# Kernel optimization log

Measured on AMD Instinct MI355X. Metric: run time of the kernel, lower is better.

The kernel has to match this reference:

```python
import jax, jax.numpy as jnp
import numpy as np

N, E, G = 50000, 800000, 64
IN, EDGE = 128, 16
HID, H = 32, 4
FHID, HF = 64, 4
OUT = 16
NEG_SLOPE = 0.2


def _segment_softmax(logits, seg, num):
    m = jax.ops.segment_max(logits, seg, num_segments=num)
    m = jnp.where(jnp.isfinite(m), m, 0.0)
    p = jnp.exp(logits - m[seg])
    s = jax.ops.segment_sum(p, seg, num_segments=num)
    return p / (s[seg] + 1e-16)


def gatv2(x, src, dst, eattr, Wl, bl, Wr, br, We, att, bias, concat):
    # PyG GATv2Conv with add_self_loops=True (edge_attr fill_value='mean')
    n = x.shape[0]
    heads, ch = att.shape
    ones = jnp.ones((src.shape[0],), x.dtype)
    cnt = jax.ops.segment_sum(ones, dst, num_segments=n)
    mean_attr = jax.ops.segment_sum(eattr, dst, num_segments=n) / jnp.maximum(cnt, 1.0)[:, None]
    loop = jnp.arange(n)
    s = jnp.concatenate([src, loop])
    d = jnp.concatenate([dst, loop])
    ea = jnp.concatenate([eattr, mean_attr], axis=0)
    xl = (x @ Wl + bl).reshape(n, heads, ch)   # lin_l (source)
    xr = (x @ Wr + br).reshape(n, heads, ch)   # lin_r (target)
    ee = (ea @ We).reshape(-1, heads, ch)      # lin_edge (no bias)
    z = jax.nn.leaky_relu(xl[s] + xr[d] + ee, NEG_SLOPE)  # [E+N, H, C]
    logits = jnp.einsum('ehc,hc->eh', z, att)
    alpha = _segment_softmax(logits, d, n)
    out = jax.ops.segment_sum(alpha[:, :, None] * xl[s], d, num_segments=n)  # [N, H, C]
    out = out.reshape(n, heads * ch) if concat else out.mean(axis=1)
    return out + bias


def _forward(x, edge_attr, src, dst, batch,
             Wl0, bl0, Wr0, br0, We0, att0, bo0,
             Wlh, blh, Wrh, brh, Weh, atth, boh,
             Wlf, blf, Wrf, brf, Wef, attf, bof,
             Wlin, blin):
    h1 = jax.nn.relu(gatv2(x, src, dst, edge_attr, Wl0, bl0, Wr0, br0, We0, att0, bo0, True))
    h2 = jax.nn.relu(gatv2(h1, src, dst, edge_attr, Wlh, blh, Wrh, brh, Weh, atth, boh, True))
    h3 = jax.nn.relu(gatv2(h2, src, dst, edge_attr, Wlf, blf, Wrf, brf, Wef, attf, bof, False))
    # global_mean_pool over graphs
    gsum = jax.ops.segment_sum(h3, batch, num_segments=G)
    gcnt = jax.ops.segment_sum(jnp.ones((h3.shape[0],), h3.dtype), batch, num_segments=G)
    g = gsum / jnp.maximum(gcnt, 1.0)[:, None]
    return g @ Wlin + blin  # final_dropout inactive in eval mode


def setup_inputs():
    key = jax.random.key(0)
    ks = jax.random.split(key, 20)
    def p(i, shape, fan_in):
        return jax.random.normal(ks[i], shape, jnp.float32) / np.sqrt(fan_in)
    z = lambda *s: jnp.zeros(s, jnp.float32)
    return {
        'x': jax.random.normal(ks[0], (N, IN), jnp.float32),
        'edge_index': jax.random.randint(ks[1], (2, E), 0, N),
        'batch': jnp.sort(jax.random.randint(ks[2], (N,), 0, G)),
        'edge_attr': jax.random.normal(ks[3], (E, EDGE), jnp.float32),
        'Wl0': p(4, (IN, H * HID), IN), 'bl0': z(H * HID),
        'Wr0': p(5, (IN, H * HID), IN), 'br0': z(H * HID),
        'We0': p(6, (EDGE, H * HID), EDGE), 'att0': p(7, (H, HID), HID), 'bo0': z(H * HID),
        'Wlh': p(8, (H * HID, H * HID), H * HID), 'blh': z(H * HID),
        'Wrh': p(9, (H * HID, H * HID), H * HID), 'brh': z(H * HID),
        'Weh': p(10, (EDGE, H * HID), EDGE), 'atth': p(11, (H, HID), HID), 'boh': z(H * HID),
        'Wlf': p(12, (H * HID, HF * FHID), H * HID), 'blf': z(HF * FHID),
        'Wrf': p(13, (H * HID, HF * FHID), H * HID), 'brf': z(HF * FHID),
        'Wef': p(14, (EDGE, HF * FHID), EDGE), 'attf': p(15, (HF, FHID), FHID), 'bof': z(FHID),
        'Wlin': p(16, (FHID, OUT), FHID), 'blin': z(OUT),
    }


def reference(x, edge_index, batch, edge_attr, Wl0, bl0, Wr0, br0, We0, att0, bo0, Wlh, blh, Wrh, brh, Weh, atth, boh, Wlf, blf, Wrf, brf, Wef, attf, bof, Wlin, blin):
    return _forward(x, edge_attr, edge_index[0], edge_index[1], batch,
                    Wl0, bl0, Wr0, br0, We0, att0, bo0,
                    Wlh, blh, Wrh, brh, Weh, atth, boh,
                    Wlf, blf, Wrf, brf, Wef, attf, bof,
                    Wlin, blin)
```

## Files before the change

### kernel.cpp

```cpp
#include <hip/hip_runtime.h>
#include <cstddef>

#define NSLOPE 0.2f

constexpr int NN = 50000;
constexpr int EE = 800000;
constexpr int GG = 64;
constexpr int SCAN_B = 1024;

typedef unsigned short ushort_t;
typedef __bf16 bhalf;
typedef bhalf bhalf8 __attribute__((ext_vector_type(8)));
typedef float floatx4 __attribute__((ext_vector_type(4)));

__device__ __forceinline__ ushort_t f2b(float f) {
  unsigned int u = __float_as_uint(f);
  unsigned int r = (u + 0x7fffu + ((u >> 16) & 1u)) >> 16;
  return (ushort_t)r;
}
__device__ __forceinline__ float b2f(ushort_t b) {
  return __uint_as_float(((unsigned int)b) << 16);
}

__global__ void hist_kernel(const int* __restrict__ dst, int* __restrict__ hist, int E) {
  int e = blockIdx.x * blockDim.x + threadIdx.x;
  if (e < E) atomicAdd(&hist[dst[e]], 1);
}

__global__ void scan_block_kernel(const int* __restrict__ in, int* __restrict__ out,
                                  int* __restrict__ bsum, int n) {
  __shared__ int tmp[SCAN_B];
  int gid = blockIdx.x * SCAN_B + threadIdx.x;
  int v = (gid < n) ? in[gid] : 0;
  tmp[threadIdx.x] = v;
  __syncthreads();
  for (int off = 1; off < SCAN_B; off <<= 1) {
    int t = (threadIdx.x >= off) ? tmp[threadIdx.x - off] : 0;
    __syncthreads();
    tmp[threadIdx.x] += t;
    __syncthreads();
  }
  if (gid < n) out[gid] = tmp[threadIdx.x];
  if (threadIdx.x == SCAN_B - 1) bsum[blockIdx.x] = tmp[threadIdx.x];
}

__global__ void scan_totals_kernel(const int* __restrict__ bsum, int* __restrict__ boff, int nb) {
  if (blockIdx.x == 0 && threadIdx.x == 0) {
    int run = 0;
    for (int i = 0; i < nb; ++i) { boff[i] = run; run += bsum[i]; }
  }
}

__global__ void add_offsets_kernel(int* __restrict__ rowptr, const int* __restrict__ boff, int n) {
  int gid = blockIdx.x * SCAN_B + threadIdx.x;
  if (gid == 0) rowptr[0] = 0;
  if (gid < n) rowptr[1 + gid] += boff[blockIdx.x];
}

__global__ void copy_cursor_kernel(const int* __restrict__ rowptr, int* __restrict__ cursor, int n) {
  int i = blockIdx.x * blockDim.x + threadIdx.x;
  if (i < n) cursor[i] = rowptr[i];
}

__global__ void scatter_perm_kernel(const int* __restrict__ dst, int* __restrict__ cursor,
                                    int* __restrict__ perm, int E) {
  int e = blockIdx.x * blockDim.x + threadIdx.x;
  if (e < E) {
    int pos = atomicAdd(&cursor[dst[e]], 1);
    perm[pos] = e;
  }
}

__global__ void permute_kernel(const int* __restrict__ perm, const int* __restrict__ src,
                               const float* __restrict__ eattr,
                               int* __restrict__ srcp, float* __restrict__ eap, int E) {
  int j = blockIdx.x * blockDim.x + threadIdx.x;
  if (j >= E) return;
  int e = perm[j];
  srcp[j] = src[e];
  const float4* a = reinterpret_cast<const float4*>(eattr + (size_t)e * 16);
  float4* b = reinterpret_cast<float4*>(eap + (size_t)j * 16);
  b[0] = a[0]; b[1] = a[1]; b[2] = a[2]; b[3] = a[3];
}

__global__ void mean_attr_kernel(const int* __restrict__ rowptr, const float* __restrict__ eap,
                                 const int* __restrict__ perm, const float* __restrict__ eattr,
                                 int usePerm, float* __restrict__ meanattr, int N) {
  int idx = blockIdx.x * blockDim.x + threadIdx.x;
  if (idx >= N * 16) return;
  int i = idx >> 4, k = idx & 15;
  int beg = rowptr[i], end = rowptr[i + 1];
  float acc = 0.f;
  if (usePerm) {
    for (int j = beg; j < end; ++j) acc += eattr[(size_t)perm[j] * 16 + k];
  } else {
    for (int j = beg; j < end; ++j) acc += eap[(size_t)j * 16 + k];
  }
  int c = end - beg; if (c < 1) c = 1;
  meanattr[idx] = acc / (float)c;
}

__global__ void f2b_kernel(const float* __restrict__ in, ushort_t* __restrict__ out, int n4) {
  int i = blockIdx.x * blockDim.x + threadIdx.x;
  if (i >= n4) return;
  float4 v = reinterpret_cast<const float4*>(in)[i];
  ushort4 o = make_ushort4(f2b(v.x), f2b(v.y), f2b(v.z), f2b(v.w));
  reinterpret_cast<ushort4*>(out)[i] = o;
}

__global__ void prep_w_kernel(const float* W0, ushort_t* T0, int n0,
                              const float* W1, ushort_t* T1, int n1,
                              const float* W2, ushort_t* T2, int n2,
                              const float* W3, ushort_t* T3, int n3,
                              const float* W4, ushort_t* T4, int n4,
                              const float* W5, ushort_t* T5, int n5) {
  const float* W; ushort_t* T; int Nc;
  switch (blockIdx.y) {
    case 0: W = W0; T = T0; Nc = n0; break;
    case 1: W = W1; T = T1; Nc = n1; break;
    case 2: W = W2; T = T2; Nc = n2; break;
    case 3: W = W3; T = T3; Nc = n3; break;
    case 4: W = W4; T = T4; Nc = n4; break;
    default: W = W5; T = T5; Nc = n5; break;
  }
  int idx = blockIdx.x * blockDim.x + threadIdx.x;
  if (idx >= Nc * 128) return;
  int n = idx >> 7, k = idx & 127;
  T[idx] = f2b(W[(size_t)k * Nc + n]);
}

__global__ __launch_bounds__(256) void gemm_bt_dual_bf16(
    const ushort_t* __restrict__ Xb,
    const ushort_t* __restrict__ Wt0, const float* __restrict__ b0, ushort_t* __restrict__ Y0,
    const ushort_t* __restrict__ Wt1, const float* __restrict__ b1, ushort_t* __restrict__ Y1,
    int M, int Nc) {
  constexpr int K = 128, BM = 128, BN = 128, LDT = 136;
  __shared__ ushort_t Als[BM * LDT];
  __shared__ ushort_t Bls[BN * LDT];
  int nb = Nc >> 7;
  int half = blockIdx.y / nb;
  int cb = blockIdx.y % nb;
  const ushort_t* Wt = half ? Wt1 : Wt0;
  const float* bias = half ? b1 : b0;
  ushort_t* Y = half ? Y1 : Y0;
  int r0 = blockIdx.x * BM;
  int col0 = cb * BN;
  int tid = threadIdx.x;
  {
    int rl = tid >> 5;
    int kq = (tid & 31) * 4;
#pragma unroll
    for (int s = 0; s < 16; ++s) {
      int row = rl + s * 8;
      int grow = r0 + row;
      ushort4 v = make_ushort4(0, 0, 0, 0);
      if (grow < M) v = *reinterpret_cast<const ushort4*>(Xb + (size_t)grow * K + kq);
      *reinterpret_cast<ushort4*>(&Als[row * LDT + kq]) = v;
      ushort4 wv = *reinterpret_cast<const ushort4*>(Wt + (size_t)(col0 + row) * K + kq);
      *reinterpret_cast<ushort4*>(&Bls[row * LDT + kq]) = wv;
    }
  }
  __syncthreads();
  int lane = tid & 63;
  int w = tid >> 6;
  int m0 = (w >> 1) * 64;
  int n0 = (w & 1) * 64;
  int rin = lane & 15, quad = lane >> 4;
  floatx4 acc[4][4];
#pragma unroll
  for (int i = 0; i < 4; ++i)
#pragma unroll
    for (int j = 0; j < 4; ++j) acc[i][j] = (floatx4){0.f, 0.f, 0.f, 0.f};
#pragma unroll
  for (int kt = 0; kt < 4; ++kt) {
    int ko = kt * 32 + quad * 8;
    bhalf8 af[4], bf[4];
#pragma unroll
    for (int i = 0; i < 4; ++i)
      af[i] = *reinterpret_cast<const bhalf8*>(&Als[(m0 + i * 16 + rin) * LDT + ko]);
#pragma unroll
    for (int i = 0; i < 4; ++i)
      bf[i] = *reinterpret_cast<const bhalf8*>(&Bls[(n0 + i * 16 + rin) * LDT + ko]);
#pragma unroll
    for (int mi = 0; mi < 4; ++mi)
#pragma unroll
      for (int ni = 0; ni < 4; ++ni)
        acc[mi][ni] = __builtin_amdgcn_mfma_f32_16x16x32_bf16(af[mi], bf[ni], acc[mi][ni], 0, 0, 0);
  }
#pragma unroll
  for (int ni = 0; ni < 4; ++ni) {
    int gcol = col0 + n0 + ni * 16 + rin;
    float bb = bias[gcol];
#pragma unroll
    for (int mi = 0; mi < 4; ++mi) {
      int growb = r0 + m0 + mi * 16 + quad * 4;
#pragma unroll
      for (int r = 0; r < 4; ++r) {
        int grow = growb + r;
        if (grow < M) Y[(size_t)grow * Nc + gcol] = f2b(acc[mi][ni][r] + bb);
      }
    }
  }
}

template <int VPL>
__device__ __forceinline__ void loadb(const ushort_t* p, float* v) {
  if constexpr (VPL == 2) {
    ushort2 t = *reinterpret_cast<const ushort2*>(p);
    v[0] = b2f(t.x); v[1] = b2f(t.y);
  } else {
    ushort4 t = *reinterpret_cast<const ushort4*>(p);
    v[0] = b2f(t.x); v[1] = b2f(t.y); v[2] = b2f(t.z); v[3] = b2f(t.w);
  }
}
template <int VPL>
__device__ __forceinline__ void storeb(ushort_t* p, const float* v) {
  if constexpr (VPL == 2) {
    *reinterpret_cast<ushort2*>(p) = make_ushort2(f2b(v[0]), f2b(v[1]));
  } else {
    *reinterpret_cast<ushort4*>(p) = make_ushort4(f2b(v[0]), f2b(v[1]), f2b(v[2]), f2b(v[3]));
  }
}

template <int VPL>
__device__ __forceinline__ float lrelu_dot(const float* xv, const float* rv,
                                           const float (*wreg)[VPL], const float* areg,
                                           const float* ea) {
  float part = 0.f;
#pragma unroll
  for (int j = 0; j < VPL; ++j) {
    float z = xv[j] + rv[j];
#pragma unroll
    for (int k = 0; k < 16; ++k) z = fmaf(ea[k], wreg[k][j], z);
    z = (z > 0.f) ? z : NSLOPE * z;
    part = fmaf(z, areg[j], part);
  }
  part += __shfl_xor(part, 1);
  part += __shfl_xor(part, 2);
  part += __shfl_xor(part, 4);
  part += __shfl_xor(part, 8);
  return part;
}

template <int EB, int VPL, int C>
__device__ __forceinline__ void process_group(
    const int* __restrict__ srcp, const float* __restrict__ eap, int j,
    const ushort_t* __restrict__ xl, int lane, const float* rv,
    const float (*wreg)[VPL], const float* areg,
    float& m, float& s, float* acc) {
  int sn[EB];
#pragma unroll
  for (int u = 0; u < EB; ++u) sn[u] = srcp[j + u];
  float xv[EB][VPL];
#pragma unroll
  for (int u = 0; u < EB; ++u) loadb<VPL>(xl + (size_t)sn[u] * C + lane * VPL, xv[u]);
  float lg[EB];
#pragma unroll
  for (int u = 0; u < EB; ++u) {
    const float* ap = eap + (size_t)(j + u) * 16;
    float ea[16];
#pragma unroll
    for (int k = 0; k < 16; ++k) ea[k] = ap[k];
    lg[u] = lrelu_dot<VPL>(xv[u], rv, wreg, areg, ea);
  }
  float newm = m;
#pragma unroll
  for (int u = 0; u < EB; ++u) newm = fmaxf(newm, lg[u]);
  float sc = __expf(m - newm);
  float p[EB], ps = 0.f;
#pragma unroll
  for (int u = 0; u < EB; ++u) { p[u] = __expf(lg[u] - newm); ps += p[u]; }
  s = fmaf(s, sc, ps);
#pragma unroll
  for (int jj = 0; jj < VPL; ++jj) {
    float t = p[0] * xv[0][jj];
#pragma unroll
    for (int u = 1; u < EB; ++u) t = fmaf(p[u], xv[u][jj], t);
    acc[jj] = fmaf(acc[jj], sc, t);
  }
  m = newm;
}

template <int VPL, int C>
__device__ __forceinline__ void process_one(
    int sn, const float* ea,
    const ushort_t* __restrict__ xl, int lane, const float* rv,
    const float (*wreg)[VPL], const float* areg,
    float& m, float& s, float* acc) {
  float xv[VPL];
  loadb<VPL>(xl + (size_t)sn * C + lane * VPL, xv);
  float lg = lrelu_dot<VPL>(xv, rv, wreg, areg, ea);
  float newm = fmaxf(m, lg);
  float sc = __expf(m - newm);
  float p = __expf(lg - newm);
  s = fmaf(s, sc, p);
#pragma unroll
  for (int jj = 0; jj < VPL; ++jj) acc[jj] = fmaf(acc[jj], sc, p * xv[jj]);
  m = newm;
}

template <int C, bool FINAL>
__global__ __launch_bounds__(256) void gat_fused_kernel(
    const int* __restrict__ rowptr,
    const int* __restrict__ srcp, const float* __restrict__ eap,
    const int* __restrict__ perm, const int* __restrict__ src,
    const float* __restrict__ eattr, const float* __restrict__ meanattr,
    int usePerm,
    const ushort_t* __restrict__ xl, const ushort_t* __restrict__ xr,
    const float* __restrict__ We,
    const float* __restrict__ att,
    const float* __restrict__ bias, ushort_t* __restrict__ hout, int N) {
  constexpr int VPL = C / 64;
  constexpr int EB = 4;
  const int lane = threadIdx.x & 63;
  int d = __builtin_amdgcn_readfirstlane(blockIdx.x * (blockDim.x >> 6) + (threadIdx.x >> 6));
  if (d >= N) return;

  float wreg[16][VPL];
  float areg[VPL];
#pragma unroll
  for (int k = 0; k < 16; ++k)
#pragma unroll
    for (int j = 0; j < VPL; ++j) wreg[k][j] = We[k * C + lane * VPL + j];
#pragma unroll
  for (int j = 0; j < VPL; ++j) areg[j] = att[lane * VPL + j];

  int beg = rowptr[d], end = rowptr[d + 1];
  float rv[VPL];
  loadb<VPL>(xr + (size_t)d * C + lane * VPL, rv);

  float m = -INFINITY, s = 0.f;
  float acc[VPL];
#pragma unroll
  for (int j = 0; j < VPL; ++j) acc[j] = 0.f;

  if (!usePerm) {
    int j = beg;
    for (; j + EB <= end; j += EB)
      process_group<EB, VPL, C>(srcp, eap, j, xl, lane, rv, wreg, areg, m, s, acc);
    for (; j < end; ++j)
      process_group<1, VPL, C>(srcp, eap, j, xl, lane, rv, wreg, areg, m, s, acc);
  } else {
    for (int j = beg; j < end; ++j) {
      int e = perm[j];
      int sn = src[e];
      const float* ap = eattr + (size_t)e * 16;
      float ea[16];
#pragma unroll
      for (int k = 0; k < 16; ++k) ea[k] = ap[k];
      process_one<VPL, C>(sn, ea, xl, lane, rv, wreg, areg, m, s, acc);
    }
  }
  {
    const float* mp = meanattr + (size_t)d * 16;
    float ea[16];
#pragma unroll
    for (int k = 0; k < 16; ++k) ea[k] = mp[k];
    process_one<VPL, C>(d, ea, xl, lane, rv, wreg, areg, m, s, acc);
  }

  float inv = 1.f / (s + 1e-16f);
  if constexpr (!FINAL) {
    float res[VPL];
#pragma unroll
    for (int j = 0; j < VPL; ++j) {
      float v = acc[j] * inv + bias[lane * VPL + j];
      res[j] = v > 0.f ? v : 0.f;
    }
    storeb<VPL>(hout + (size_t)d * C + lane * VPL, res);
  } else {
    float v[VPL];
#pragma unroll
    for (int j = 0; j < VPL; ++j) v[j] = acc[j] * inv;
#pragma unroll
    for (int j = 0; j < VPL; ++j) {
      v[j] += __shfl_xor(v[j], 16);
      v[j] += __shfl_xor(v[j], 32);
    }
    if (lane < 16) {
      float res[VPL];
#pragma unroll
      for (int j = 0; j < VPL; ++j) {
        float val = 0.25f * v[j] + bias[lane * VPL + j];
        res[j] = val > 0.f ? val : 0.f;
      }
      storeb<VPL>(hout + (size_t)d * 64 + lane * VPL, res);
    }
  }
}

__global__ __launch_bounds__(256) void pool_kernel(
    const ushort_t* __restrict__ h3, const int* __restrict__ batch,
    float* __restrict__ gsum, float* __restrict__ gcnt, int N) {
  const int lane = threadIdx.x & 63;
  const int w = blockIdx.x * (blockDim.x >> 6) + (threadIdx.x >> 6);
  const int nw = gridDim.x * (blockDim.x >> 6);
  const int chunk = (N + nw - 1) / nw;
  int i0 = w * chunk;
  int i1 = i0 + chunk; if (i1 > N) i1 = N;
  if (i0 >= i1) return;
  int cur = batch[i0];
  float acc = 0.f;
  int cnt = 0;
  for (int i = i0; i < i1; ++i) {
    int g = batch[i];
    if (g != cur) {
      atomicAdd(&gsum[(size_t)cur * 64 + lane], acc);
      if (lane == 0) atomicAdd(&gcnt[cur], (float)cnt);
      acc = 0.f; cnt = 0; cur = g;
    }
    acc += b2f(h3[(size_t)i * 64 + lane]);
    ++cnt;
  }
  atomicAdd(&gsum[(size_t)cur * 64 + lane], acc);
  if (lane == 0) atomicAdd(&gcnt[cur], (float)cnt);
}

__global__ void final_kernel(const float* __restrict__ gsum, const float* __restrict__ gcnt,
                             const float* __restrict__ Wlin, const float* __restrict__ blin,
                             float* __restrict__ out) {
  int idx = blockIdx.x * blockDim.x + threadIdx.x;
  if (idx >= GG * 16) return;
  int g = idx >> 4, o = idx & 15;
  float c = gcnt[g];
  c = c > 1.f ? c : 1.f;
  float inv = 1.f / c;
  float acc = blin[o];
  for (int f = 0; f < 64; ++f) acc = fmaf(gsum[(size_t)g * 64 + f] * inv, Wlin[f * 16 + o], acc);
  out[idx] = acc;
}

extern "C" void kernel_launch(void* const* d_in, const int* in_sizes, int n_in,
                              void* d_out, int out_size, void* d_ws, size_t ws_size,
                              hipStream_t stream) {
  (void)in_sizes; (void)n_in; (void)out_size;
  const float* x     = (const float*)d_in[0];
  const int*   eidx  = (const int*)d_in[1];
  const int*   batch = (const int*)d_in[2];
  const float* eattr = (const float*)d_in[3];
  const float* Wl0 = (const float*)d_in[4];  const float* bl0 = (const float*)d_in[5];
  const float* Wr0 = (const float*)d_in[6];  const float* br0 = (const float*)d_in[7];
  const float* We0 = (const float*)d_in[8];  const float* att0 = (const float*)d_in[9];
  const float* bo0 = (const float*)d_in[10];
  const float* Wlh = (const float*)d_in[11]; const float* blh = (const float*)d_in[12];
  const float* Wrh = (const float*)d_in[13]; const float* brh = (const float*)d_in[14];
  const float* Weh = (const float*)d_in[15]; const float* atth = (const float*)d_in[16];
  const float* boh = (const float*)d_in[17];
  const float* Wlf = (const float*)d_in[18]; const float* blf = (const float*)d_in[19];
  const float* Wrf = (const float*)d_in[20]; const float* brf = (const float*)d_in[21];
  const float* Wef = (const float*)d_in[22]; const float* attf = (const float*)d_in[23];
  const float* bof = (const float*)d_in[24];
  const float* Wlin = (const float*)d_in[25]; const float* blin = (const float*)d_in[26];

  const int* src = eidx;
  const int* dst = eidx + EE;

  char* ws = (char*)d_ws;
  size_t off = 0;
  auto take = [&](size_t bytes) -> void* {
    void* p = ws + off;
    off += (bytes + 1023) & ~(size_t)1023;
    return p;
  };
  ushort_t* xl     = (ushort_t*)take((size_t)NN * 256 * 2);
  ushort_t* xr     = (ushort_t*)take((size_t)NN * 256 * 2);
  ushort_t* hb     = (ushort_t*)take((size_t)NN * 128 * 2);
  ushort_t* xb     = (ushort_t*)take((size_t)NN * 128 * 2);
  float* meanattr  = (float*)take((size_t)NN * 16 * 4);
  int* hist        = (int*)take((size_t)NN * 4);
  int* rowptr      = (int*)take((size_t)(NN + 1) * 4);
  int* cursor      = (int*)take((size_t)NN * 4);
  int* perm        = (int*)take((size_t)EE * 4);
  int* bsum        = (int*)take(256);
  int* boff        = (int*)take(256);
  float* gsum      = (float*)take((size_t)GG * 64 * 4);
  float* gcnt      = (float*)take((size_t)GG * 4);
  ushort_t* wtl0   = (ushort_t*)take((size_t)128 * 128 * 2);
  ushort_t* wtr0   = (ushort_t*)take((size_t)128 * 128 * 2);
  ushort_t* wtlh   = (ushort_t*)take((size_t)128 * 128 * 2);
  ushort_t* wtrh   = (ushort_t*)take((size_t)128 * 128 * 2);
  ushort_t* wtlf   = (ushort_t*)take((size_t)256 * 128 * 2);
  ushort_t* wtrf   = (ushort_t*)take((size_t)256 * 128 * 2);
  size_t perm_need = off + (((size_t)EE * 4 + 1023) & ~(size_t)1023)
                   + (((size_t)EE * 16 * 4 + 1023) & ~(size_t)1023);
  int usePerm = (ws_size >= perm_need) ? 0 : 1;
  int* srcp = nullptr; float* eap = nullptr;
  if (!usePerm) {
    srcp = (int*)take((size_t)EE * 4);
    eap  = (float*)take((size_t)EE * 16 * 4);
  }

  hipMemsetAsync(hist, 0, (size_t)NN * 4, stream);
  hipMemsetAsync(gsum, 0, (size_t)GG * 64 * 4, stream);
  hipMemsetAsync(gcnt, 0, (size_t)GG * 4, stream);
  hist_kernel<<<(EE + 255) / 256, 256, 0, stream>>>(dst, hist, EE);
  int nsb = (NN + SCAN_B - 1) / SCAN_B;
  scan_block_kernel<<<nsb, SCAN_B, 0, stream>>>(hist, rowptr + 1, bsum, NN);
  scan_totals_kernel<<<1, 64, 0, stream>>>(bsum, boff, nsb);
  add_offsets_kernel<<<nsb, SCAN_B, 0, stream>>>(rowptr, boff, NN);
  copy_cursor_kernel<<<(NN + 255) / 256, 256, 0, stream>>>(rowptr, cursor, NN);
  scatter_perm_kernel<<<(EE + 255) / 256, 256, 0, stream>>>(dst, cursor, perm, EE);
  if (!usePerm)
    permute_kernel<<<(EE + 255) / 256, 256, 0, stream>>>(perm, src, eattr, srcp, eap, EE);
  mean_attr_kernel<<<(NN * 16 + 255) / 256, 256, 0, stream>>>(rowptr, eap, perm, eattr,
                                                              usePerm, meanattr, NN);
  prep_w_kernel<<<dim3(128, 6), 256, 0, stream>>>(Wl0, wtl0, 128, Wr0, wtr0, 128,
                                                  Wlh, wtlh, 128, Wrh, wtrh, 128,
                                                  Wlf, wtlf, 256, Wrf, wtrf, 256);
  f2b_kernel<<<(NN * 128 / 4 + 255) / 256, 256, 0, stream>>>(x, xb, NN * 128 / 4);

  const int AGG_BLOCKS = (NN + 3) / 4;
  const int GEMM_MB = (NN + 127) / 128;

  gemm_bt_dual_bf16<<<dim3(GEMM_MB, 2), 256, 0, stream>>>(xb, wtl0, bl0, xl, wtr0, br0, xr, NN, 128);
  gat_fused_kernel<128, false><<<AGG_BLOCKS, 256, 0, stream>>>(
      rowptr, srcp, eap, perm, src, eattr, meanattr, usePerm, xl, xr, We0, att0, bo0, hb, NN);
  gemm_bt_dual_bf16<<<dim3(GEMM_MB, 2), 256, 0, stream>>>(hb, wtlh, blh, xl, wtrh, brh, xr, NN, 128);
  gat_fused_kernel<128, false><<<AGG_BLOCKS, 256, 0, stream>>>(
      rowptr, srcp, eap, perm, src, eattr, meanattr, usePerm, xl, xr, Weh, atth, boh, hb, NN);
  gemm_bt_dual_bf16<<<dim3(GEMM_MB, 4), 256, 0, stream>>>(hb, wtlf, blf, xl, wtrf, brf, xr, NN, 256);
  gat_fused_kernel<256, true><<<AGG_BLOCKS, 256, 0, stream>>>(
      rowptr, srcp, eap, perm, src, eattr, meanattr, usePerm, xl, xr, Wef, attf, bof, hb, NN);
  pool_kernel<<<128, 256, 0, stream>>>(hb, batch, gsum, gcnt, NN);
  final_kernel<<<4, 256, 0, stream>>>(gsum, gcnt, Wlin, blin, (float*)d_out);
}
```

Measured before the change: 776.4 us.

## Store edge attributes as packed fp16 and use fdot2 for edge projection

Permuted edge attributes and per-node mean attributes are now stored as packed half2 pairs, which halves the bytes each aggregation kernel streams per edge. The per-edge 16-term edge projection uses the v_dot2 fp16 instruction against half2-packed We weights held in registers, cutting the FMA count. Longer edge batches (8 edges for C=128) and a 2-edge tail path are added to expose more memory-level parallelism. The cost is reduced precision in edge attributes and weights, plus higher register pressure from the larger batches.

```diff
diff --git a/kernel.cpp b/kernel.cpp
--- a/kernel.cpp
+++ b/kernel.cpp
@@ -9,9 +9,12 @@
 constexpr int SCAN_B = 1024;
 
 typedef unsigned short ushort_t;
+typedef unsigned int uint_t;
 typedef __bf16 bhalf;
 typedef bhalf bhalf8 __attribute__((ext_vector_type(8)));
 typedef float floatx4 __attribute__((ext_vector_type(4)));
+typedef _Float16 half_t;
+typedef half_t half2_t __attribute__((ext_vector_type(2)));
 
 __device__ __forceinline__ ushort_t f2b(float f) {
   unsigned int u = __float_as_uint(f);
@@ -20,6 +23,18 @@
 }
 __device__ __forceinline__ float b2f(ushort_t b) {
   return __uint_as_float(((unsigned int)b) << 16);
+}
+__device__ __forceinline__ uint_t packh2(float a, float b) {
+  half2_t h = {(half_t)a, (half_t)b};
+  return __builtin_bit_cast(uint_t, h);
+}
+__device__ __forceinline__ float dot2acc(uint_t ea, half2_t w, float c) {
+  half2_t a = __builtin_bit_cast(half2_t, ea);
+#if __has_builtin(__builtin_amdgcn_fdot2)
+  return __builtin_amdgcn_fdot2(a, w, c, false);
+#else
+  return c + (float)a.x * (float)w.x + (float)a.y * (float)w.y;
+#endif
 }
 
 __global__ void hist_kernel(const int* __restrict__ dst, int* __restrict__ hist, int E) {
@@ -73,31 +88,42 @@
 
 __global__ void permute_kernel(const int* __restrict__ perm, const int* __restrict__ src,
                                const float* __restrict__ eattr,
-                               int* __restrict__ srcp, float* __restrict__ eap, int E) {
+                               int* __restrict__ srcp, uint_t* __restrict__ eah, int E) {
   int j = blockIdx.x * blockDim.x + threadIdx.x;
   if (j >= E) return;
   int e = perm[j];
   srcp[j] = src[e];
-  const float4* a = reinterpret_cast<const float4*>(eattr + (size_t)e * 16);
-  float4* b = reinterpret_cast<float4*>(eap + (size_t)j * 16);
-  b[0] = a[0]; b[1] = a[1]; b[2] = a[2]; b[3] = a[3];
-}
-
-__global__ void mean_attr_kernel(const int* __restrict__ rowptr, const float* __restrict__ eap,
+  const float* a = eattr + (size_t)e * 16;
+  uint_t o[8];
+#pragma unroll
+  for (int k2 = 0; k2 < 8; ++k2) o[k2] = packh2(a[2 * k2], a[2 * k2 + 1]);
+  uint4* b = reinterpret_cast<uint4*>(eah + (size_t)j * 8);
+  b[0] = make_uint4(o[0], o[1], o[2], o[3]);
+  b[1] = make_uint4(o[4], o[5], o[6], o[7]);
+}
+
+__global__ void mean_attr_kernel(const int* __restrict__ rowptr, const uint_t* __restrict__ eah,
                                  const int* __restrict__ perm, const float* __restrict__ eattr,
-                                 int usePerm, float* __restrict__ meanattr, int N) {
+                                 int usePerm, uint_t* __restrict__ meanattr_h, int N) {
   int idx = blockIdx.x * blockDim.x + threadIdx.x;
-  if (idx >= N * 16) return;
-  int i = idx >> 4, k = idx & 15;
+  if (idx >= N * 8) return;
+  int i = idx >> 3, k2 = idx & 7;
   int beg = rowptr[i], end = rowptr[i + 1];
-  float acc = 0.f;
-  if (usePerm) {
-    for (int j = beg; j < end; ++j) acc += eattr[(size_t)perm[j] * 16 + k];
+  float ax = 0.f, ay = 0.f;
+  if (!usePerm) {
+    for (int j = beg; j < end; ++j) {
+      half2_t h = __builtin_bit_cast(half2_t, eah[(size_t)j * 8 + k2]);
+      ax += (float)h.x; ay += (float)h.y;
+    }
   } else {
-    for (int j = beg; j < end; ++j) acc += eap[(size_t)j * 16 + k];
+    for (int j = beg; j < end; ++j) {
+      const float* ap = eattr + (size_t)perm[j] * 16 + k2 * 2;
+      ax += ap[0]; ay += ap[1];
+    }
   }
   int c = end - beg; if (c < 1) c = 1;
-  meanattr[idx] = acc / (float)c;
+  float inv = 1.f / (float)c;
+  meanattr_h[idx] = packh2(ax * inv, ay * inv);
 }
 
 __global__ void f2b_kernel(const float* __restrict__ in, ushort_t* __restrict__ out, int n4) {
@@ -224,16 +250,16 @@
 
 template <int VPL>
 __device__ __forceinline__ float lrelu_dot(const float* xv, const float* rv,
-                                           const float (*wreg)[VPL], const float* areg,
-                                           const float* ea) {
+                                           const half2_t (*wepk)[VPL], const float* areg,
+                                           const uint_t* ea) {
   float part = 0.f;
 #pragma unroll
   for (int j = 0; j < VPL; ++j) {
     float z = xv[j] + rv[j];
 #pragma unroll
-    for (int k = 0; k < 16; ++k) z = fmaf(ea[k], wreg[k][j], z);
-    z = (z > 0.f) ? z : NSLOPE * z;
-    part = fmaf(z, areg[j], part);
+    for (int k2 = 0; k2 < 8; ++k2) z = dot2acc(ea[k2], wepk[k2][j], z);
+    float zl = fmaxf(z, NSLOPE * z);
+    part = fmaf(zl, areg[j], part);
   }
   part += __shfl_xor(part, 1);
   part += __shfl_xor(part, 2);
@@ -244,9 +270,9 @@
 
 template <int EB, int VPL, int C>
 __device__ __forceinline__ void process_group(
-    const int* __restrict__ srcp, const float* __restrict__ eap, int j,
+    const int* __restrict__ srcp, const uint_t* __restrict__ eah, int j,
     const ushort_t* __restrict__ xl, int lane, const float* rv,
-    const float (*wreg)[VPL], const float* areg,
+    const half2_t (*wepk)[VPL], const float* areg,
     float& m, float& s, float* acc) {
   int sn[EB];
 #pragma unroll
@@ -257,11 +283,11 @@
   float lg[EB];
 #pragma unroll
   for (int u = 0; u < EB; ++u) {
-    const float* ap = eap + (size_t)(j + u) * 16;
-    float ea[16];
-#pragma unroll
-    for (int k = 0; k < 16; ++k) ea[k] = ap[k];
-    lg[u] = lrelu_dot<VPL>(xv[u], rv, wreg, areg, ea);
+    const uint_t* ap = eah + (size_t)(j + u) * 8;
+    uint_t ea[8];
+#pragma unroll
+    for (int k2 = 0; k2 < 8; ++k2) ea[k2] = ap[k2];
+    lg[u] = lrelu_dot<VPL>(xv[u], rv, wepk, areg, ea);
   }
   float newm = m;
 #pragma unroll
@@ -282,14 +308,14 @@
 }
 
 template <int VPL, int C>
-__device__ __forceinline__ void process_one(
-    int sn, const float* ea,
+__device__ __forceinline__ void process_edge(
+    int sn, const uint_t* ea,
     const ushort_t* __restrict__ xl, int lane, const float* rv,
-    const float (*wreg)[VPL], const float* areg,
+    const half2_t (*wepk)[VPL], const float* areg,
     float& m, float& s, float* acc) {
   float xv[VPL];
   loadb<VPL>(xl + (size_t)sn * C + lane * VPL, xv);
-  float lg = lrelu_dot<VPL>(xv, rv, wreg, areg, ea);
+  float lg = lrelu_dot<VPL>(xv, rv, wepk, areg, ea);
   float newm = fmaxf(m, lg);
   float sc = __expf(m - newm);
   float p = __expf(lg - newm);
@@ -302,26 +328,28 @@
 template <int C, bool FINAL>
 __global__ __launch_bounds__(256) void gat_fused_kernel(
     const int* __restrict__ rowptr,
-    const int* __restrict__ srcp, const float* __restrict__ eap,
+    const int* __restrict__ srcp, const uint_t* __restrict__ eah,
     const int* __restrict__ perm, const int* __restrict__ src,
-    const float* __restrict__ eattr, const float* __restrict__ meanattr,
+    const float* __restrict__ eattr, const uint_t* __restrict__ meanattr_h,
     int usePerm,
     const ushort_t* __restrict__ xl, const ushort_t* __restrict__ xr,
     const float* __restrict__ We,
     const float* __restrict__ att,
     const float* __restrict__ bias, ushort_t* __restrict__ hout, int N) {
   constexpr int VPL = C / 64;
-  constexpr int EB = 4;
   const int lane = threadIdx.x & 63;
   int d = __builtin_amdgcn_readfirstlane(blockIdx.x * (blockDim.x >> 6) + (threadIdx.x >> 6));
   if (d >= N) return;
 
-  float wreg[16][VPL];
+  half2_t wepk[8][VPL];
   float areg[VPL];
 #pragma unroll
-  for (int k = 0; k < 16; ++k)
-#pragma unroll
-    for (int j = 0; j < VPL; ++j) wreg[k][j] = We[k * C + lane * VPL + j];
+  for (int k2 = 0; k2 < 8; ++k2)
+#pragma unroll
+    for (int j = 0; j < VPL; ++j) {
+      int ch = lane * VPL + j;
+      wepk[k2][j] = (half2_t){(half_t)We[(2 * k2) * C + ch], (half_t)We[(2 * k2 + 1) * C + ch]};
+    }
 #pragma unroll
   for (int j = 0; j < VPL; ++j) areg[j] = att[lane * VPL + j];
 
@@ -336,27 +364,33 @@
 
   if (!usePerm) {
     int j = beg;
-    for (; j + EB <= end; j += EB)
-      process_group<EB, VPL, C>(srcp, eap, j, xl, lane, rv, wreg, areg, m, s, acc);
+    if constexpr (C == 128) {
+      for (; j + 8 <= end; j += 8)
+        process_group<8, VPL, C>(srcp, eah, j, xl, lane, rv, wepk, areg, m, s, acc);
+    }
+    for (; j + 4 <= end; j += 4)
+      process_group<4, VPL, C>(srcp, eah, j, xl, lane, rv, wepk, areg, m, s, acc);
+    for (; j + 2 <= end; j += 2)
+      process_group<2, VPL, C>(srcp, eah, j, xl, lane, rv, wepk, areg, m, s, acc);
     for (; j < end; ++j)
-      process_group<1, VPL, C>(srcp, eap, j, xl, lane, rv, wreg, areg, m, s, acc);
+      process_group<1, VPL, C>(srcp, eah, j, xl, lane, rv, wepk, areg, m, s, acc);
   } else {
     for (int j = beg; j < end; ++j) {
       int e = perm[j];
       int sn = src[e];
       const float* ap = eattr + (size_t)e * 16;
-      float ea[16];
-#pragma unroll
-      for (int k = 0; k < 16; ++k) ea[k] = ap[k];
-      process_one<VPL, C>(sn, ea, xl, lane, rv, wreg, areg, m, s, acc);
+      uint_t ea[8];
+#pragma unroll
+      for (int k2 = 0; k2 < 8; ++k2) ea[k2] = packh2(ap[2 * k2], ap[2 * k2 + 1]);
+      process_edge<VPL, C>(sn, ea, xl, lane, rv, wepk, areg, m, s, acc);
     }
   }
   {
-    const float* mp = meanattr + (size_t)d * 16;
-    float ea[16];
-#pragma unroll
-    for (int k = 0; k < 16; ++k) ea[k] = mp[k];
-    process_one<VPL, C>(d, ea, xl, lane, rv, wreg, areg, m, s, acc);
+    const uint_t* mp = meanattr_h + (size_t)d * 8;
+    uint_t ea[8];
+#pragma unroll
+    for (int k2 = 0; k2 < 8; ++k2) ea[k2] = mp[k2];
+    process_edge<VPL, C>(d, ea, xl, lane, rv, wepk, areg, m, s, acc);
   }
 
   float inv = 1.f / (s + 1e-16f);
@@ -466,7 +500,7 @@
   ushort_t* xr     = (ushort_t*)take((size_t)NN * 256 * 2);
   ushort_t* hb     = (ushort_t*)take((size_t)NN * 128 * 2);
   ushort_t* xb     = (ushort_t*)take((size_t)NN * 128 * 2);
-  float* meanattr  = (float*)take((size_t)NN * 16 * 4);
+  uint_t* meanattr_h = (uint_t*)take((size_t)NN * 8 * 4);
   int* hist        = (int*)take((size_t)NN * 4);
   int* rowptr      = (int*)take((size_t)(NN + 1) * 4);
   int* cursor      = (int*)take((size_t)NN * 4);
@@ -482,12 +516,12 @@
   ushort_t* wtlf   = (ushort_t*)take((size_t)256 * 128 * 2);
   ushort_t* wtrf   = (ushort_t*)take((size_t)256 * 128 * 2);
   size_t perm_need = off + (((size_t)EE * 4 + 1023) & ~(size_t)1023)
-                   + (((size_t)EE * 16 * 4 + 1023) & ~(size_t)1023);
+                   + (((size_t)EE * 8 * 4 + 1023) & ~(size_t)1023);
   int usePerm = (ws_size >= perm_need) ? 0 : 1;
-  int* srcp = nullptr; float* eap = nullptr;
+  int* srcp = nullptr; uint_t* eah = nullptr;
   if (!usePerm) {
     srcp = (int*)take((size_t)EE * 4);
-    eap  = (float*)take((size_t)EE * 16 * 4);
+    eah  = (uint_t*)take((size_t)EE * 8 * 4);
   }
 
   hipMemsetAsync(hist, 0, (size_t)NN * 4, stream);
@@ -501,9 +535,9 @@
   copy_cursor_kernel<<<(NN + 255) / 256, 256, 0, stream>>>(rowptr, cursor, NN);
   scatter_perm_kernel<<<(EE + 255) / 256, 256, 0, stream>>>(dst, cursor, perm, EE);
   if (!usePerm)
-    permute_kernel<<<(EE + 255) / 256, 256, 0, stream>>>(perm, src, eattr, srcp, eap, EE);
-  mean_attr_kernel<<<(NN * 16 + 255) / 256, 256, 0, stream>>>(rowptr, eap, perm, eattr,
-                                                              usePerm, meanattr, NN);
+    permute_kernel<<<(EE + 255) / 256, 256, 0, stream>>>(perm, src, eattr, srcp, eah, EE);
+  mean_attr_kernel<<<(NN * 8 + 255) / 256, 256, 0, stream>>>(rowptr, eah, perm, eattr,
+                                                             usePerm, meanattr_h, NN);
   prep_w_kernel<<<dim3(128, 6), 256, 0, stream>>>(Wl0, wtl0, 128, Wr0, wtr0, 128,
                                                   Wlh, wtlh, 128, Wrh, wtrh, 128,
                                                   Wlf, wtlf, 256, Wrf, wtrf, 256);
@@ -514,13 +548,13 @@
 
   gemm_bt_dual_bf16<<<dim3(GEMM_MB, 2), 256, 0, stream>>>(xb, wtl0, bl0, xl, wtr0, br0, xr, NN, 128);
   gat_fused_kernel<128, false><<<AGG_BLOCKS, 256, 0, stream>>>(
-      rowptr, srcp, eap, perm, src, eattr, meanattr, usePerm, xl, xr, We0, att0, bo0, hb, NN);
+      rowptr, srcp, eah, perm, src, eattr, meanattr_h, usePerm, xl, xr, We0, att0, bo0, hb, NN);
   gemm_bt_dual_bf16<<<dim3(GEMM_MB, 2), 256, 0, stream>>>(hb, wtlh, blh, xl, wtrh, brh, xr, NN, 128);
   gat_fused_kernel<128, false><<<AGG_BLOCKS, 256, 0, stream>>>(
-      rowptr, srcp, eap, perm, src, eattr, meanattr, usePerm, xl, xr, Weh, atth, boh, hb, NN);
+      rowptr, srcp, eah, perm, src, eattr, meanattr_h, usePerm, xl, xr, Weh, atth, boh, hb, NN);
   gemm_bt_dual_bf16<<<dim3(GEMM_MB, 4), 256, 0, stream>>>(hb, wtlf, blf, xl, wtrf, brf, xr, NN, 256);
   gat_fused_kernel<256, true><<<AGG_BLOCKS, 256, 0, stream>>>(
-      rowptr, srcp, eap, perm, src, eattr, meanattr, usePerm, xl, xr, Wef, attf, bof, hb, NN);
+      rowptr, srcp, eah, perm, src, eattr, meanattr_h, usePerm, xl, xr, Wef, attf, bof, hb, NN);
   pool_kernel<<<128, 256, 0, stream>>>(hb, batch, gsum, gcnt, NN);
   final_kernel<<<4, 256, 0, stream>>>(gsum, gcnt, Wlin, blin, (float*)d_out);
 }
```

Result: faster. 727.8 us (-6.3%).

## Compute edge projections with MFMA in GAT aggregation and store edge attrs as fp16

Applied to the files above, without the earlier changes.

The per-edge lin_edge projection (16×C FMAs per lane) moves out of the aggregation loop. Each wave now processes 16 edges at a time with an f16 MFMA, stages the results in shared memory, and reads them back per edge. Edge attributes are permuted into CSR order directly in the scatter kernel and stored as fp16, which halves their traffic and removes the separate permute kernel and the usePerm fallback. The cost is fp16 rounding of edge attributes and projections, extra LDS traffic, and MFMA work wasted on partially filled edge tiles.

```diff
diff --git a/kernel.cpp b/kernel.cpp
--- a/kernel.cpp
+++ b/kernel.cpp
@@ -9,9 +9,13 @@
 constexpr int SCAN_B = 1024;
 
 typedef unsigned short ushort_t;
+typedef unsigned int uint_t;
 typedef __bf16 bhalf;
 typedef bhalf bhalf8 __attribute__((ext_vector_type(8)));
 typedef float floatx4 __attribute__((ext_vector_type(4)));
+typedef _Float16 half_t;
+typedef half_t half2_t __attribute__((ext_vector_type(2)));
+typedef half_t half8_t __attribute__((ext_vector_type(8)));
 
 __device__ __forceinline__ ushort_t f2b(float f) {
   unsigned int u = __float_as_uint(f);
@@ -20,6 +24,10 @@
 }
 __device__ __forceinline__ float b2f(ushort_t b) {
   return __uint_as_float(((unsigned int)b) << 16);
+}
+__device__ __forceinline__ uint_t packh2(float a, float b) {
+  half2_t h = {(half_t)a, (half_t)b};
+  return __builtin_bit_cast(uint_t, h);
 }
 
 __global__ void hist_kernel(const int* __restrict__ dst, int* __restrict__ hist, int E) {
@@ -62,42 +70,32 @@
   if (i < n) cursor[i] = rowptr[i];
 }
 
-__global__ void scatter_perm_kernel(const int* __restrict__ dst, int* __restrict__ cursor,
-                                    int* __restrict__ perm, int E) {
+__global__ void scatter_all_kernel(const int* __restrict__ dst, const int* __restrict__ src,
+                                   const float* __restrict__ eattr, int* __restrict__ cursor,
+                                   int* __restrict__ srcp, half_t* __restrict__ eab, int E) {
   int e = blockIdx.x * blockDim.x + threadIdx.x;
-  if (e < E) {
-    int pos = atomicAdd(&cursor[dst[e]], 1);
-    perm[pos] = e;
-  }
-}
-
-__global__ void permute_kernel(const int* __restrict__ perm, const int* __restrict__ src,
-                               const float* __restrict__ eattr,
-                               int* __restrict__ srcp, float* __restrict__ eap, int E) {
-  int j = blockIdx.x * blockDim.x + threadIdx.x;
-  if (j >= E) return;
-  int e = perm[j];
-  srcp[j] = src[e];
-  const float4* a = reinterpret_cast<const float4*>(eattr + (size_t)e * 16);
-  float4* b = reinterpret_cast<float4*>(eap + (size_t)j * 16);
-  b[0] = a[0]; b[1] = a[1]; b[2] = a[2]; b[3] = a[3];
-}
-
-__global__ void mean_attr_kernel(const int* __restrict__ rowptr, const float* __restrict__ eap,
-                                 const int* __restrict__ perm, const float* __restrict__ eattr,
-                                 int usePerm, float* __restrict__ meanattr, int N) {
+  if (e >= E) return;
+  int pos = atomicAdd(&cursor[dst[e]], 1);
+  srcp[pos] = src[e];
+  const float* a = eattr + (size_t)e * 16;
+  uint_t o[8];
+#pragma unroll
+  for (int k2 = 0; k2 < 8; ++k2) o[k2] = packh2(a[2 * k2], a[2 * k2 + 1]);
+  uint4* b = reinterpret_cast<uint4*>(eab + (size_t)pos * 16);
+  b[0] = make_uint4(o[0], o[1], o[2], o[3]);
+  b[1] = make_uint4(o[4], o[5], o[6], o[7]);
+}
+
+__global__ void mean_attr_kernel(const int* __restrict__ rowptr, const half_t* __restrict__ eab,
+                                 half_t* __restrict__ mab, int N) {
   int idx = blockIdx.x * blockDim.x + threadIdx.x;
   if (idx >= N * 16) return;
   int i = idx >> 4, k = idx & 15;
   int beg = rowptr[i], end = rowptr[i + 1];
-  float acc = 0.f;
-  if (usePerm) {
-    for (int j = beg; j < end; ++j) acc += eattr[(size_t)perm[j] * 16 + k];
-  } else {
-    for (int j = beg; j < end; ++j) acc += eap[(size_t)j * 16 + k];
-  }
+  float a = 0.f;
+  for (int j = beg; j < end; ++j) a += (float)eab[(size_t)j * 16 + k];
   int c = end - beg; if (c < 1) c = 1;
-  meanattr[idx] = acc / (float)c;
+  mab[idx] = (half_t)(a / (float)c);
 }
 
 __global__ void f2b_kernel(const float* __restrict__ in, ushort_t* __restrict__ out, int n4) {
@@ -129,14 +127,29 @@
   T[idx] = f2b(W[(size_t)k * Nc + n]);
 }
 
+__global__ void prep_we_kernel(const float* W0, half_t* T0,
+                               const float* W1, half_t* T1,
+                               const float* W2, half_t* T2) {
+  const float* W; half_t* T; int Cc;
+  switch (blockIdx.y) {
+    case 0: W = W0; T = T0; Cc = 128; break;
+    case 1: W = W1; T = T1; Cc = 128; break;
+    default: W = W2; T = T2; Cc = 256; break;
+  }
+  int idx = blockIdx.x * blockDim.x + threadIdx.x;
+  if (idx >= Cc * 16) return;
+  int c = idx >> 4, k = idx & 15;
+  T[idx] = (half_t)W[(size_t)k * Cc + c];
+}
+
 __global__ __launch_bounds__(256) void gemm_bt_dual_bf16(
     const ushort_t* __restrict__ Xb,
     const ushort_t* __restrict__ Wt0, const float* __restrict__ b0, ushort_t* __restrict__ Y0,
     const ushort_t* __restrict__ Wt1, const float* __restrict__ b1, ushort_t* __restrict__ Y1,
     int M, int Nc) {
-  constexpr int K = 128, BM = 128, BN = 128, LDT = 136;
+  constexpr int K = 128, BM = 128, LDT = 136;
   __shared__ ushort_t Als[BM * LDT];
-  __shared__ ushort_t Bls[BN * LDT];
+  __shared__ ushort_t Bls[BM * LDT];
   int nb = Nc >> 7;
   int half = blockIdx.y / nb;
   int cb = blockIdx.y % nb;
@@ -144,7 +157,7 @@
   const float* bias = half ? b1 : b0;
   ushort_t* Y = half ? Y1 : Y0;
   int r0 = blockIdx.x * BM;
-  int col0 = cb * BN;
+  int col0 = cb * 128;
   int tid = threadIdx.x;
   {
     int rl = tid >> 5;
@@ -222,111 +235,36 @@
   }
 }
 
-template <int VPL>
-__device__ __forceinline__ float lrelu_dot(const float* xv, const float* rv,
-                                           const float (*wreg)[VPL], const float* areg,
-                                           const float* ea) {
-  float part = 0.f;
-#pragma unroll
-  for (int j = 0; j < VPL; ++j) {
-    float z = xv[j] + rv[j];
-#pragma unroll
-    for (int k = 0; k < 16; ++k) z = fmaf(ea[k], wreg[k][j], z);
-    z = (z > 0.f) ? z : NSLOPE * z;
-    part = fmaf(z, areg[j], part);
-  }
-  part += __shfl_xor(part, 1);
-  part += __shfl_xor(part, 2);
-  part += __shfl_xor(part, 4);
-  part += __shfl_xor(part, 8);
-  return part;
-}
-
-template <int EB, int VPL, int C>
-__device__ __forceinline__ void process_group(
-    const int* __restrict__ srcp, const float* __restrict__ eap, int j,
-    const ushort_t* __restrict__ xl, int lane, const float* rv,
-    const float (*wreg)[VPL], const float* areg,
-    float& m, float& s, float* acc) {
-  int sn[EB];
-#pragma unroll
-  for (int u = 0; u < EB; ++u) sn[u] = srcp[j + u];
-  float xv[EB][VPL];
-#pragma unroll
-  for (int u = 0; u < EB; ++u) loadb<VPL>(xl + (size_t)sn[u] * C + lane * VPL, xv[u]);
-  float lg[EB];
-#pragma unroll
-  for (int u = 0; u < EB; ++u) {
-    const float* ap = eap + (size_t)(j + u) * 16;
-    float ea[16];
-#pragma unroll
-    for (int k = 0; k < 16; ++k) ea[k] = ap[k];
-    lg[u] = lrelu_dot<VPL>(xv[u], rv, wreg, areg, ea);
-  }
-  float newm = m;
-#pragma unroll
-  for (int u = 0; u < EB; ++u) newm = fmaxf(newm, lg[u]);
-  float sc = __expf(m - newm);
-  float p[EB], ps = 0.f;
-#pragma unroll
-  for (int u = 0; u < EB; ++u) { p[u] = __expf(lg[u] - newm); ps += p[u]; }
-  s = fmaf(s, sc, ps);
-#pragma unroll
-  for (int jj = 0; jj < VPL; ++jj) {
-    float t = p[0] * xv[0][jj];
-#pragma unroll
-    for (int u = 1; u < EB; ++u) t = fmaf(p[u], xv[u][jj], t);
-    acc[jj] = fmaf(acc[jj], sc, t);
-  }
-  m = newm;
-}
-
-template <int VPL, int C>
-__device__ __forceinline__ void process_one(
-    int sn, const float* ea,
-    const ushort_t* __restrict__ xl, int lane, const float* rv,
-    const float (*wreg)[VPL], const float* areg,
-    float& m, float& s, float* acc) {
-  float xv[VPL];
-  loadb<VPL>(xl + (size_t)sn * C + lane * VPL, xv);
-  float lg = lrelu_dot<VPL>(xv, rv, wreg, areg, ea);
-  float newm = fmaxf(m, lg);
-  float sc = __expf(m - newm);
-  float p = __expf(lg - newm);
-  s = fmaf(s, sc, p);
-#pragma unroll
-  for (int jj = 0; jj < VPL; ++jj) acc[jj] = fmaf(acc[jj], sc, p * xv[jj]);
-  m = newm;
-}
-
 template <int C, bool FINAL>
-__global__ __launch_bounds__(256) void gat_fused_kernel(
-    const int* __restrict__ rowptr,
-    const int* __restrict__ srcp, const float* __restrict__ eap,
-    const int* __restrict__ perm, const int* __restrict__ src,
-    const float* __restrict__ eattr, const float* __restrict__ meanattr,
-    int usePerm,
+__global__ __launch_bounds__(256) void gat_mfma_kernel(
+    const int* __restrict__ rowptr, const int* __restrict__ srcp,
+    const half_t* __restrict__ eab,
+    const half_t* __restrict__ mab,
+    const half_t* __restrict__ Web,
     const ushort_t* __restrict__ xl, const ushort_t* __restrict__ xr,
-    const float* __restrict__ We,
-    const float* __restrict__ att,
-    const float* __restrict__ bias, ushort_t* __restrict__ hout, int N) {
+    const float* __restrict__ att, const float* __restrict__ bias,
+    ushort_t* __restrict__ hout, int N) {
   constexpr int VPL = C / 64;
-  constexpr int EB = 4;
-  const int lane = threadIdx.x & 63;
-  int d = __builtin_amdgcn_readfirstlane(blockIdx.x * (blockDim.x >> 6) + (threadIdx.x >> 6));
+  constexpr int ROW = C + 4;
+  __shared__ ushort_t WebL[C * 32];
+  __shared__ half_t eeL[4][16 * ROW];
+  const int tid = threadIdx.x;
+  for (int i = tid; i < C * 32; i += 256) {
+    int c = i >> 5, k = i & 31;
+    WebL[i] = (k < 16) ? reinterpret_cast<const ushort_t*>(Web)[c * 16 + k] : (ushort_t)0;
+  }
+  __syncthreads();
+  const int lane = tid & 63;
+  const int wv = tid >> 6;
+  const int rin = lane & 15, quad = lane >> 4;
+  int d = __builtin_amdgcn_readfirstlane(blockIdx.x * 4 + wv);
   if (d >= N) return;
-
-  float wreg[16][VPL];
-  float areg[VPL];
-#pragma unroll
-  for (int k = 0; k < 16; ++k)
-#pragma unroll
-    for (int j = 0; j < VPL; ++j) wreg[k][j] = We[k * C + lane * VPL + j];
+  half_t* eeW = &eeL[wv][0];
+
+  float areg[VPL], rv[VPL];
 #pragma unroll
   for (int j = 0; j < VPL; ++j) areg[j] = att[lane * VPL + j];
-
   int beg = rowptr[d], end = rowptr[d + 1];
-  float rv[VPL];
   loadb<VPL>(xr + (size_t)d * C + lane * VPL, rv);
 
   float m = -INFINITY, s = 0.f;
@@ -334,29 +272,78 @@
 #pragma unroll
   for (int j = 0; j < VPL; ++j) acc[j] = 0.f;
 
-  if (!usePerm) {
-    int j = beg;
-    for (; j + EB <= end; j += EB)
-      process_group<EB, VPL, C>(srcp, eap, j, xl, lane, rv, wreg, areg, m, s, acc);
-    for (; j < end; ++j)
-      process_group<1, VPL, C>(srcp, eap, j, xl, lane, rv, wreg, areg, m, s, acc);
-  } else {
-    for (int j = beg; j < end; ++j) {
-      int e = perm[j];
-      int sn = src[e];
-      const float* ap = eattr + (size_t)e * 16;
-      float ea[16];
-#pragma unroll
-      for (int k = 0; k < 16; ++k) ea[k] = ap[k];
-      process_one<VPL, C>(sn, ea, xl, lane, rv, wreg, areg, m, s, acc);
-    }
-  }
-  {
-    const float* mp = meanattr + (size_t)d * 16;
-    float ea[16];
-#pragma unroll
-    for (int k = 0; k < 16; ++k) ea[k] = mp[k];
-    process_one<VPL, C>(d, ea, xl, lane, rv, wreg, areg, m, s, acc);
+  for (int j0 = beg; j0 <= end; j0 += 16) {
+    int arow = j0 + rin;
+    const half_t* abase = (arow == end) ? (mab + (size_t)d * 16) : (eab + (size_t)arow * 16);
+    half8_t af;
+#pragma unroll
+    for (int i = 0; i < 8; ++i) af[i] = (half_t)0.f;
+    if (quad < 2) af = *reinterpret_cast<const half8_t*>(abase + quad * 8);
+#pragma unroll
+    for (int t = 0; t < C / 16; ++t) {
+      half8_t bf = *reinterpret_cast<const half8_t*>(&WebL[(t * 16 + rin) * 32 + quad * 8]);
+      floatx4 dd = __builtin_amdgcn_mfma_f32_16x16x32_f16(af, bf, (floatx4){0.f, 0.f, 0.f, 0.f},
+                                                          0, 0, 0);
+#pragma unroll
+      for (int r = 0; r < 4; ++r)
+        eeW[(quad * 4 + r) * ROW + t * 16 + rin] = (half_t)dd[r];
+    }
+    int vmax = end + 1 - j0; if (vmax > 16) vmax = 16;
+    for (int u0 = 0; u0 < vmax; u0 += 4) {
+      int sn[4];
+      float xv[4][VPL], ee[4][VPL], lg[4];
+#pragma unroll
+      for (int u = 0; u < 4; ++u) {
+        int idx = j0 + u0 + u;
+        sn[u] = (idx < end) ? srcp[idx] : d;
+      }
+#pragma unroll
+      for (int u = 0; u < 4; ++u) loadb<VPL>(xl + (size_t)sn[u] * C + lane * VPL, xv[u]);
+#pragma unroll
+      for (int u = 0; u < 4; ++u) {
+        const half_t* ep = eeW + (u0 + u) * ROW + lane * VPL;
+        if constexpr (VPL == 2) {
+          half2_t h = *reinterpret_cast<const half2_t*>(ep);
+          ee[u][0] = (float)h.x; ee[u][1] = (float)h.y;
+        } else {
+          half2_t h0 = *reinterpret_cast<const half2_t*>(ep);
+          half2_t h1 = *reinterpret_cast<const half2_t*>(ep + 2);
+          ee[u][0] = (float)h0.x; ee[u][1] = (float)h0.y;
+          ee[u][2] = (float)h1.x; ee[u][3] = (float)h1.y;
+        }
+      }
+#pragma unroll
+      for (int u = 0; u < 4; ++u) {
+        float part = 0.f;
+#pragma unroll
+        for (int j = 0; j < VPL; ++j) {
+          float z = xv[u][j] + rv[j] + ee[u][j];
+          float zl = fmaxf(z, NSLOPE * z);
+          part = fmaf(zl, areg[j], part);
+        }
+        part += __shfl_xor(part, 1);
+        part += __shfl_xor(part, 2);
+        part += __shfl_xor(part, 4);
+        part += __shfl_xor(part, 8);
+        lg[u] = (j0 + u0 + u <= end) ? part : -INFINITY;
+      }
+      float newm = m;
+#pragma unroll
+      for (int u = 0; u < 4; ++u) newm = fmaxf(newm, lg[u]);
+      float sc = __expf(m - newm);
+      float p[4], ps = 0.f;
+#pragma unroll
+      for (int u = 0; u < 4; ++u) { p[u] = __expf(lg[u] - newm); ps += p[u]; }
+      s = fmaf(s, sc, ps);
+#pragma unroll
+      for (int jj = 0; jj < VPL; ++jj) {
+        float t = p[0] * xv[0][jj];
+#pragma unroll
+        for (int u = 1; u < 4; ++u) t = fmaf(p[u], xv[u][jj], t);
+        acc[jj] = fmaf(acc[jj], sc, t);
+      }
+      m = newm;
+    }
   }
 
   float inv = 1.f / (s + 1e-16f);
@@ -433,7 +420,7 @@
 extern "C" void kernel_launch(void* const* d_in, const int* in_sizes, int n_in,
                               void* d_out, int out_size, void* d_ws, size_t ws_size,
                               hipStream_t stream) {
-  (void)in_sizes; (void)n_in; (void)out_size;
+  (void)in_sizes; (void)n_in; (void)out_size; (void)ws_size;
   const float* x     = (const float*)d_in[0];
   const int*   eidx  = (const int*)d_in[1];
   const int*   batch = (const int*)d_in[2];
@@ -462,33 +449,29 @@
     off += (bytes + 1023) & ~(size_t)1023;
     return p;
   };
-  ushort_t* xl     = (ushort_t*)take((size_t)NN * 256 * 2);
-  ushort_t* xr     = (ushort_t*)take((size_t)NN * 256 * 2);
-  ushort_t* hb     = (ushort_t*)take((size_t)NN * 128 * 2);
-  ushort_t* xb     = (ushort_t*)take((size_t)NN * 128 * 2);
-  float* meanattr  = (float*)take((size_t)NN * 16 * 4);
-  int* hist        = (int*)take((size_t)NN * 4);
-  int* rowptr      = (int*)take((size_t)(NN + 1) * 4);
-  int* cursor      = (int*)take((size_t)NN * 4);
-  int* perm        = (int*)take((size_t)EE * 4);
-  int* bsum        = (int*)take(256);
-  int* boff        = (int*)take(256);
-  float* gsum      = (float*)take((size_t)GG * 64 * 4);
-  float* gcnt      = (float*)take((size_t)GG * 4);
-  ushort_t* wtl0   = (ushort_t*)take((size_t)128 * 128 * 2);
-  ushort_t* wtr0   = (ushort_t*)take((size_t)128 * 128 * 2);
-  ushort_t* wtlh   = (ushort_t*)take((size_t)128 * 128 * 2);
-  ushort_t* wtrh   = (ushort_t*)take((size_t)128 * 128 * 2);
-  ushort_t* wtlf   = (ushort_t*)take((size_t)256 * 128 * 2);
-  ushort_t* wtrf   = (ushort_t*)take((size_t)256 * 128 * 2);
-  size_t perm_need = off + (((size_t)EE * 4 + 1023) & ~(size_t)1023)
-                   + (((size_t)EE * 16 * 4 + 1023) & ~(size_t)1023);
-  int usePerm = (ws_size >= perm_need) ? 0 : 1;
-  int* srcp = nullptr; float* eap = nullptr;
-  if (!usePerm) {
-    srcp = (int*)take((size_t)EE * 4);
-    eap  = (float*)take((size_t)EE * 16 * 4);
-  }
+  ushort_t* xl   = (ushort_t*)take((size_t)NN * 256 * 2);
+  ushort_t* xr   = (ushort_t*)take((size_t)NN * 256 * 2);
+  ushort_t* hb   = (ushort_t*)take((size_t)NN * 128 * 2);
+  ushort_t* xb   = (ushort_t*)take((size_t)NN * 128 * 2);
+  half_t* eab    = (half_t*)take((size_t)(EE + 16) * 16 * 2);
+  half_t* mab    = (half_t*)take((size_t)NN * 16 * 2);
+  int* srcp      = (int*)take((size_t)(EE + 16) * 4);
+  int* hist      = (int*)take((size_t)NN * 4);
+  int* rowptr    = (int*)take((size_t)(NN + 1) * 4);
+  int* cursor    = (int*)take((size_t)NN * 4);
+  int* bsum      = (int*)take(256);
+  int* boff      = (int*)take(256);
+  float* gsum    = (float*)take((size_t)GG * 64 * 4);
+  float* gcnt    = (float*)take((size_t)GG * 4);
+  ushort_t* wtl0 = (ushort_t*)take((size_t)128 * 128 * 2);
+  ushort_t* wtr0 = (ushort_t*)take((size_t)128 * 128 * 2);
+  ushort_t* wtlh = (ushort_t*)take((size_t)128 * 128 * 2);
+  ushort_t* wtrh = (ushort_t*)take((size_t)128 * 128 * 2);
+  ushort_t* wtlf = (ushort_t*)take((size_t)256 * 128 * 2);
+  ushort_t* wtrf = (ushort_t*)take((size_t)256 * 128 * 2);
+  half_t* web0   = (half_t*)take((size_t)128 * 16 * 2);
+  half_t* webh   = (half_t*)take((size_t)128 * 16 * 2);
+  half_t* webf   = (half_t*)take((size_t)256 * 16 * 2);
 
   hipMemsetAsync(hist, 0, (size_t)NN * 4, stream);
   hipMemsetAsync(gsum, 0, (size_t)GG * 64 * 4, stream);
@@ -499,28 +482,26 @@
   scan_totals_kernel<<<1, 64, 0, stream>>>(bsum, boff, nsb);
   add_offsets_kernel<<<nsb, SCAN_B, 0, stream>>>(rowptr, boff, NN);
   copy_cursor_kernel<<<(NN + 255) / 256, 256, 0, stream>>>(rowptr, cursor, NN);
-  scatter_perm_kernel<<<(EE + 255) / 256, 256, 0, stream>>>(dst, cursor, perm, EE);
-  if (!usePerm)
-    permute_kernel<<<(EE + 255) / 256, 256, 0, stream>>>(perm, src, eattr, srcp, eap, EE);
-  mean_attr_kernel<<<(NN * 16 + 255) / 256, 256, 0, stream>>>(rowptr, eap, perm, eattr,
-                                                              usePerm, meanattr, NN);
+  scatter_all_kernel<<<(EE + 255) / 256, 256, 0, stream>>>(dst, src, eattr, cursor, srcp, eab, EE);
+  mean_attr_kernel<<<(NN * 16 + 255) / 256, 256, 0, stream>>>(rowptr, eab, mab, NN);
   prep_w_kernel<<<dim3(128, 6), 256, 0, stream>>>(Wl0, wtl0, 128, Wr0, wtr0, 128,
                                                   Wlh, wtlh, 128, Wrh, wtrh, 128,
                                                   Wlf, wtlf, 256, Wrf, wtrf, 256);
+  prep_we_kernel<<<dim3(16, 3), 256, 0, stream>>>(We0, web0, Weh, webh, Wef, webf);
   f2b_kernel<<<(NN * 128 / 4 + 255) / 256, 256, 0, stream>>>(x, xb, NN * 128 / 4);
 
   const int AGG_BLOCKS = (NN + 3) / 4;
   const int GEMM_MB = (NN + 127) / 128;
 
   gemm_bt_dual_bf16<<<dim3(GEMM_MB, 2), 256, 0, stream>>>(xb, wtl0, bl0, xl, wtr0, br0, xr, NN, 128);
-  gat_fused_kernel<128, false><<<AGG_BLOCKS, 256, 0, stream>>>(
-      rowptr, srcp, eap, perm, src, eattr, meanattr, usePerm, xl, xr, We0, att0, bo0, hb, NN);
+  gat_mfma_kernel<128, false><<<AGG_BLOCKS, 256, 0, stream>>>(
+      rowptr, srcp, eab, mab, web0, xl, xr, att0, bo0, hb, NN);
   gemm_bt_dual_bf16<<<dim3(GEMM_MB, 2), 256, 0, stream>>>(hb, wtlh, blh, xl, wtrh, brh, xr, NN, 128);
-  gat_fused_kernel<128, false><<<AGG_BLOCKS, 256, 0, stream>>>(
-      rowptr, srcp, eap, perm, src, eattr, meanattr, usePerm, xl, xr, Weh, atth, boh, hb, NN);
+  gat_mfma_kernel<128, false><<<AGG_BLOCKS, 256, 0, stream>>>(
+      rowptr, srcp, eab, mab, webh, xl, xr, atth, boh, hb, NN);
   gemm_bt_dual_bf16<<<dim3(GEMM_MB, 4), 256, 0, stream>>>(hb, wtlf, blf, xl, wtrf, brf, xr, NN, 256);
-  gat_fused_kernel<256, true><<<AGG_BLOCKS, 256, 0, stream>>>(
-      rowptr, srcp, eap, perm, src, eattr, meanattr, usePerm, xl, xr, Wef, attf, bof, hb, NN);
+  gat_mfma_kernel<256, true><<<AGG_BLOCKS, 256, 0, stream>>>(
+      rowptr, srcp, eab, mab, webf, xl, xr, attf, bof, hb, NN);
   pool_kernel<<<128, 256, 0, stream>>>(hb, batch, gsum, gcnt, NN);
   final_kernel<<<4, 256, 0, stream>>>(gsum, gcnt, Wlin, blin, (float*)d_out);
 }
```

After: 934.1 us. 1.2x slower.
